# Kernel optimization log

Hardware: AMD Instinct MI355X
Metric: run time of the kernel (lower is better)

Reference implementation:

```python
import jax, jax.numpy as jnp
import numpy as np


def setup_inputs() -> dict:
    key = jax.random.key(0)
    ks = jax.random.split(key, 24)
    N, C, D_IN, HID, EMB = 8192, 4096, 32, 128, 128
    s = 0.05
    inp = {
        "cand_feat": jax.random.normal(ks[0], (1, C, D_IN), jnp.float32),
        "graph_pos": jax.random.uniform(ks[1], (N, 3), jnp.float32),
        "graph_rad": jax.random.uniform(ks[2], (N,), jnp.float32) + 0.01,
        "L": jnp.ones((1,), jnp.float32),
        "adj": jax.random.uniform(ks[3], (N, N), jnp.float32),
        "mask": jax.random.randint(ks[4], (1, C), 0, 2, jnp.int32),
        # candidate encoder: 32 -> 128 -> 128
        "cW1": jax.random.normal(ks[5], (D_IN, 128), jnp.float32) * s,
        "cb1": jnp.zeros((128,), jnp.float32),
        "cW2": jax.random.normal(ks[6], (128, EMB), jnp.float32) * s,
        "cb2": jnp.zeros((EMB,), jnp.float32),
        # graph encoder input proj: 4 -> 128
        "gW0": jax.random.normal(ks[7], (4, HID), jnp.float32) * s,
        "gb0": jnp.zeros((HID,), jnp.float32),
        # 3 GNN layers: concat(2*HID) -> HID
        "gnnW": jax.random.normal(ks[8], (3, 2 * HID, HID), jnp.float32) * s,
        "gnnb": jnp.zeros((3, HID), jnp.float32),
        # output proj: 2*HID -> EMB
        "goW": jax.random.normal(ks[9], (2 * HID, EMB), jnp.float32) * s,
        "gob": jnp.zeros((EMB,), jnp.float32),
        # fusion: 2*EMB -> 256 -> 128 -> 1
        "fW1": jax.random.normal(ks[10], (2 * EMB, 256), jnp.float32) * s,
        "fb1": jnp.zeros((256,), jnp.float32),
        "fW2": jax.random.normal(ks[11], (256, 128), jnp.float32) * s,
        "fb2": jnp.zeros((128,), jnp.float32),
        "fW3": jax.random.normal(ks[12], (128, 1), jnp.float32) * s,
        "fb3": jnp.zeros((1,), jnp.float32),
    }
    return inp


def reference(cand_feat, graph_pos, graph_rad, L, adj, mask,
              cW1, cb1, cW2, cb2, gW0, gb0, gnnW, gnnb, goW, gob,
              fW1, fb1, fW2, fb2, fW3, fb3):
    relu = jax.nn.relu
    # ---- candidate encoder: [1, C, 32] -> [1, C, 128]
    cand_emb = relu(relu(cand_feat @ cW1 + cb1) @ cW2 + cb2)
    # ---- graph encoder ----
    node = jnp.concatenate([graph_pos / L, (graph_rad / jnp.max(graph_rad))[:, None]], axis=1)  # [N, 4]
    h = relu(node @ gW0 + gb0)  # [N, HID]
    deg = jnp.clip(jnp.sum(adj, axis=-1, keepdims=True), 1.0)  # [N, 1]
    for i in range(gnnW.shape[0]):
        agg = (adj @ h) / deg                       # degree-normalized aggregation
        h = relu(jnp.concatenate([h, agg], axis=-1) @ gnnW[i] + gnnb[i])
    h_glob = jnp.concatenate([jnp.max(h, axis=0), jnp.mean(h, axis=0)], axis=-1)  # [2*HID]
    graph_emb = h_glob @ goW + gob  # [EMB]
    # ---- fusion decoder ----
    g_exp = jnp.broadcast_to(graph_emb[None, None, :], cand_emb.shape)
    combined = jnp.concatenate([cand_emb, g_exp], axis=-1)  # [1, C, 2*EMB]
    scores = (relu(relu(combined @ fW1 + fb1) @ fW2 + fb2) @ fW3 + fb3)[..., 0]  # [1, C]
    return jnp.where(mask == 0, -jnp.inf, scores)
```

## Files before the change

### kernel.cpp

```cpp
#include <hip/hip_runtime.h>
#include <hip/hip_bf16.h>

constexpr int NN  = 8192;
constexpr int CC  = 4096;
constexpr int HD  = 128;
constexpr int KSPLIT = 8;
constexpr int KCHUNK = NN / KSPLIT;
constexpr int NKP_CHUNK = KCHUNK / 64;
constexpr int NKP_TOT = NN / 64;
constexpr int CCH = 32;

typedef __attribute__((ext_vector_type(4))) float f32x4;

static __device__ __forceinline__ unsigned short f2bf(float f) {
  unsigned int u = __builtin_bit_cast(unsigned int, f);
  unsigned int lsb = (u >> 16) & 1u;
  u += 0x7fffu + lsb;
  return (unsigned short)(u >> 16);
}
static __device__ __forceinline__ float bf2f(unsigned short u) {
  return __builtin_bit_cast(float, ((unsigned int)u) << 16);
}
static __device__ __forceinline__ float e4m3f(unsigned char b) {
  unsigned e = (b >> 3) & 0xF, m = b & 7;
  if (e) return __builtin_bit_cast(float, ((e + 120u) << 23) | (m << 20));
  return (float)m * 0.001953125f;
}
static __device__ __forceinline__ unsigned long long rfl64(unsigned long long x) {
  unsigned int lo = __builtin_amdgcn_readfirstlane((unsigned int)x);
  unsigned int hi = __builtin_amdgcn_readfirstlane((unsigned int)(x >> 32));
  return ((unsigned long long)hi << 32) | lo;
}

static __device__ __forceinline__ size_t pidx8(int t16, int kbp, int lane) {
  return (((size_t)t16 * NKP_TOT + kbp) * 64 + lane) * 16;
}

__global__ __launch_bounds__(256) void k_radmax(const float* __restrict__ rad, float* out) {
  __shared__ float red[256];
  int t = threadIdx.x;
  float m = 0.0f;
  for (int i = t; i < NN; i += 256) m = fmaxf(m, rad[i]);
  red[t] = m; __syncthreads();
  for (int s = 128; s > 0; s >>= 1) {
    if (t < s) red[t] = fmaxf(red[t], red[t + s]);
    __syncthreads();
  }
  if (t == 0) out[0] = red[0];
}

__global__ __launch_bounds__(256) void k_h0(const float* __restrict__ pos, const float* __restrict__ rad,
                                            const float* __restrict__ Lp, const float* __restrict__ rmax,
                                            const float* __restrict__ gW0, const float* __restrict__ gb0,
                                            float* __restrict__ h, unsigned char* __restrict__ h8) {
  __shared__ __align__(8) unsigned char lt8[128][80];
  int t = threadIdx.x;
  int i0 = blockIdx.x * 64;
  float invL = 1.0f / Lp[0];
  float invR = 1.0f / rmax[0];
  for (int rep = 0; rep < 32; ++rep) {
    int idx = rep * 256 + t;
    int il = idx >> 7, j = idx & 127;
    int i = i0 + il;
    float n0 = pos[i * 3 + 0] * invL, n1 = pos[i * 3 + 1] * invL, n2 = pos[i * 3 + 2] * invL;
    float n3 = rad[i] * invR;
    float v = gb0[j] + n0 * gW0[j] + n1 * gW0[128 + j] + n2 * gW0[256 + j] + n3 * gW0[384 + j];
    v = fmaxf(v, 0.0f);
    h[(size_t)i * HD + j] = v;
    int enc = __builtin_amdgcn_cvt_pk_fp8_f32(v, 0.0f, 0, false);
    lt8[j][il] = (unsigned char)(enc & 0xFF);
  }
  __syncthreads();
  const int lane = t & 63, w = t >> 6;
  #pragma unroll
  for (int it = 0; it < 2; ++it) {
    int t16 = it * 4 + w;
    int j = t16 * 16 + (lane & 15);
    int ib = (lane >> 4) * 8;
    unsigned long long lo = *(const unsigned long long*)(&lt8[j][ib]);
    unsigned long long hi = *(const unsigned long long*)(&lt8[j][ib + 32]);
    uint4 q;
    q.x = (unsigned)lo; q.y = (unsigned)(lo >> 32);
    q.z = (unsigned)hi; q.w = (unsigned)(hi >> 32);
    *(uint4*)(h8 + pidx8(t16, blockIdx.x, lane)) = q;
  }
}

__global__ __launch_bounds__(256) void k_convP8(const float* __restrict__ adj,
                                                unsigned char* __restrict__ adjP8,
                                                float* __restrict__ pd) {
  __shared__ __align__(8) unsigned char lt[64 * 256];
  const int t = threadIdx.x;
  const int r0 = blockIdx.x * 64;
  const int c0 = blockIdx.y * 256;
  const int l = t & 63, w = t >> 6;
  #pragma unroll
  for (int p = 0; p < 16; ++p) {
    int r = p * 4 + w;
    int c = l * 4;
    float4 v = *(const float4*)(adj + (size_t)(r0 + r) * NN + c0 + c);
    int b32 = __builtin_amdgcn_cvt_pk_fp8_f32(v.x, v.y, 0, false);
    b32 = __builtin_amdgcn_cvt_pk_fp8_f32(v.z, v.w, b32, true);
    int g = l >> 1;
    int addr = r * 256 + ((g ^ (r & 7)) << 3) + ((l & 1) * 4);
    *(unsigned int*)(lt + addr) = (unsigned int)b32;
  }
  __syncthreads();
  {
    int r = t >> 2, qd = t & 3;
    float s = 0.f;
    #pragma unroll
    for (int k8 = 0; k8 < 8; ++k8) {
      int g = qd * 8 + k8;
      int addr = r * 256 + ((g ^ (r & 7)) << 3);
      unsigned long long v = *(const unsigned long long*)(lt + addr);
      #pragma unroll
      for (int b = 0; b < 8; ++b) s += e4m3f((unsigned char)(v >> (b * 8)));
    }
    s += __shfl_xor(s, 1);
    s += __shfl_xor(s, 2);
    if (qd == 0) pd[(size_t)blockIdx.y * NN + r0 + r] = s;
  }
  #pragma unroll
  for (int it = 0; it < 4; ++it) {
    int chunk = it * 4 + w;
    int t16l = chunk >> 2, kbpl = chunk & 3;
    int r = t16l * 16 + (l & 15);
    int cb0 = kbpl * 64 + (l >> 4) * 8;
    int g0 = cb0 >> 3, g1 = g0 + 4;
    unsigned long long lo = *(const unsigned long long*)(lt + r * 256 + ((g0 ^ (r & 7)) << 3));
    unsigned long long hi = *(const unsigned long long*)(lt + r * 256 + ((g1 ^ (r & 7)) << 3));
    uint4 q;
    q.x = (unsigned)lo; q.y = (unsigned)(lo >> 32);
    q.z = (unsigned)hi; q.w = (unsigned)(hi >> 32);
    *(uint4*)(adjP8 + pidx8(blockIdx.x * 4 + t16l, (c0 >> 6) + kbpl, l)) = q;
  }
}

__global__ __launch_bounds__(256) void k_degsum(const float* __restrict__ pd, float* __restrict__ deg) {
  int i = blockIdx.x * 256 + threadIdx.x;
  float s = 0.f;
  #pragma unroll
  for (int c = 0; c < CCH; ++c) s += pd[(size_t)c * NN + i];
  deg[i] = fmaxf(s, 1.0f);
}

#define MM32(SA_, SB_) {                                                    \
  _Pragma("unroll")                                                         \
  for (int i = 0; i < 4; ++i) {                                             \
    union { uint4 q; long long ll[2]; } ua; ua.q = SA_[i];                  \
    _Pragma("unroll")                                                       \
    for (int j = 0; j < 4; ++j) {                                           \
      union { uint4 q; long long ll[2]; } ub; ub.q = SB_[j];                \
      acc[i][j] = __builtin_amdgcn_mfma_f32_16x16x32_fp8_fp8(               \
          ua.ll[0], ub.ll[0], acc[i][j], 0, 0, 0);                          \
    } }                                                                     \
  _Pragma("unroll")                                                         \
  for (int i = 0; i < 4; ++i) {                                             \
    union { uint4 q; long long ll[2]; } ua; ua.q = SA_[i];                  \
    _Pragma("unroll")                                                       \
    for (int j = 0; j < 4; ++j) {                                           \
      union { uint4 q; long long ll[2]; } ub; ub.q = SB_[j];                \
      acc[i][j] = __builtin_amdgcn_mfma_f32_16x16x32_fp8_fp8(               \
          ua.ll[1], ub.ll[1], acc[i][j], 0, 0, 0);                          \
    } } }

#define GLD(dst, base, imm)                                               \
  asm volatile("global_load_dwordx4 %0, %1, %2 offset:" #imm              \
               : "=v"(dst) : "v"(voff), "s"(base))
#define WAITV(n) do { asm volatile("s_waitcnt vmcnt(" #n ")");            \
                      __builtin_amdgcn_sched_barrier(0); } while (0)

__global__ __launch_bounds__(256) void k_gemmP(const unsigned char* __restrict__ AP,
                                               const unsigned char* __restrict__ h8,
                                               unsigned short* __restrict__ part) {
  __shared__ __align__(16) char smem[32768];
  const int t = threadIdx.x, lane = t & 63, w = t >> 6;
  const int bm = blockIdx.x, ks = blockIdx.y;
  const int kb0p = ks * NKP_CHUNK;
  const int lr = lane & 15, kg = lane >> 4;
  const int wr = w >> 1, wc = w & 1;
  const unsigned int voff = (unsigned int)(lane * 16);

  unsigned long long bA[4], bB[4];
  #pragma unroll
  for (int q = 0; q < 4; ++q) {
    bA[q] = rfl64((unsigned long long)(AP + pidx8(bm * 8 + wr * 4 + q, kb0p, 0)));
    bB[q] = rfl64((unsigned long long)(h8 + pidx8(wc * 4 + q, kb0p, 0)));
  }

  f32x4 acc[4][4];
  #pragma unroll
  for (int i = 0; i < 4; ++i)
    #pragma unroll
    for (int j = 0; j < 4; ++j) acc[i][j] = f32x4{0.f, 0.f, 0.f, 0.f};

  uint4 S0a[4], S0b[4], S1a[4], S1b[4], S2a[4], S2b[4], S3a[4], S3b[4];

  #pragma unroll
  for (int q = 0; q < 4; ++q) { GLD(S0a[q], bA[q], 0); GLD(S0b[q], bB[q], 0); }
  #pragma unroll
  for (int q = 0; q < 4; ++q) { GLD(S1a[q], bA[q], 1024); GLD(S1b[q], bB[q], 1024); }
  #pragma unroll
  for (int q = 0; q < 4; ++q) { GLD(S2a[q], bA[q], 2048); GLD(S2b[q], bB[q], 2048); }

#define PHASE(CA, CB, NA, NB)                                             \
  do {                                                                    \
    _Pragma("unroll")                                                     \
    for (int q = 0; q < 4; ++q) { GLD(NA[q], bA[q], 3072);                \
                                  GLD(NB[q], bB[q], 3072); }              \
    _Pragma("unroll")                                                     \
    for (int q = 0; q < 4; ++q) { bA[q] += 1024; bB[q] += 1024; }         \
    WAITV(24);                                                            \
    MM32(CA, CB);                                                        \
    __builtin_amdgcn_sched_barrier(0);                                    \
  } while (0)

  for (int r = 0; r < 3; ++r) {
    PHASE(S0a, S0b, S3a, S3b);
    PHASE(S1a, S1b, S0a, S0b);
    PHASE(S2a, S2b, S1a, S1b);
    PHASE(S3a, S3b, S2a, S2b);
  }
  PHASE(S0a, S0b, S3a, S3b);
  WAITV(16);
  MM32(S1a, S1b);
  __builtin_amdgcn_sched_barrier(0);
  WAITV(8);
  MM32(S2a, S2b);
  __builtin_amdgcn_sched_barrier(0);
  WAITV(0);
  MM32(S3a, S3b);
#undef PHASE

  __syncthreads();
  unsigned short* pl = (unsigned short*)smem;
  #pragma unroll
  for (int i = 0; i < 4; ++i)
    #pragma unroll
    for (int j = 0; j < 4; ++j)
      #pragma unroll
      for (int jj = 0; jj < 4; ++jj)
        pl[(wr * 64 + i * 16 + kg * 4 + jj) * 128 + wc * 64 + j * 16 + lr] =
            f2bf(acc[i][j][jj]);
  __syncthreads();
  uint4* gout = (uint4*)(part + (size_t)ks * NN * HD + (size_t)bm * 128 * HD);
  const uint4* ls = (const uint4*)smem;
  #pragma unroll
  for (int k = 0; k < 8; ++k) gout[k * 256 + t] = ls[k * 256 + t];
}

__global__ __launch_bounds__(256) void k_update(const unsigned short* __restrict__ part,
                                                const float* __restrict__ deg,
                                                const float* __restrict__ hin,
                                                const float* __restrict__ W, const float* __restrict__ bias,
                                                float* __restrict__ hout, unsigned char* __restrict__ h8,
                                                int last) {
  __shared__ float cc[16][256];
  __shared__ __align__(8) unsigned char lt2[128][24];
  int t = threadIdx.x;
  int r0 = blockIdx.x * 16;
  for (int rep = 0; rep < 8; ++rep) {
    int idx = rep * 256 + t;
    int rl = idx >> 7, j = idx & 127;
    int row = r0 + rl;
    float s = 0.f;
    for (int ks = 0; ks < KSPLIT; ++ks)
      s += bf2f(part[((size_t)ks * NN + row) * HD + j]);
    cc[rl][128 + j] = s / deg[row];
    cc[rl][j] = hin[(size_t)row * HD + j];
  }
  __syncthreads();
  int jo = t & 127, rbase = t >> 7;
  float accv[8];
  float bj = bias[jo];
  for (int rr = 0; rr < 8; ++rr) accv[rr] = bj;
  for (int jj = 0; jj < 256; ++jj) {
    float wv = W[jj * HD + jo];
    for (int rr = 0; rr < 8; ++rr) accv[rr] += cc[rbase + rr * 2][jj] * wv;
  }
  for (int rr = 0; rr < 8; ++rr) {
    int rl = rbase + rr * 2;
    float v = fmaxf(accv[rr], 0.f);
    hout[(size_t)(r0 + rl) * HD + jo] = v;
    if (!last) {
      int enc = __builtin_amdgcn_cvt_pk_fp8_f32(v, 0.0f, 0, false);
      lt2[jo][rl] = (unsigned char)(enc & 0xFF);
    }
  }
  if (!last) {
    __syncthreads();
    const int q = (r0 >> 4) & 3;
    const int kbp = r0 >> 6;
    #pragma unroll
    for (int it = 0; it < 2; ++it) {
      int idx = it * 256 + t;
      int lane = idx & 63, t16 = (it * 256 + t) >> 6;
      int g = lane >> 4;
      if ((g >> 1) == (q & 1)) {
        int j = t16 * 16 + (lane & 15);
        unsigned long long v = *(const unsigned long long*)(&lt2[j][(g & 1) * 8]);
        *(unsigned long long*)(h8 + pidx8(t16, kbp, lane) + (q >> 1) * 8) = v;
      }
    }
  }
}

__global__ __launch_bounds__(256) void k_pool(const float* __restrict__ h,
                                              float* __restrict__ pmax, float* __restrict__ psum) {
  int b = blockIdx.x, t = threadIdx.x;
  int j = t & 127, half = t >> 7;
  int r0 = b * 128 + half * 64;
  float mx = -1e30f, sm = 0.f;
  for (int r = r0; r < r0 + 64; ++r) {
    float v = h[(size_t)r * HD + j];
    mx = fmaxf(mx, v); sm += v;
  }
  __shared__ float lm[2][128], ls[2][128];
  lm[half][j] = mx; ls[half][j] = sm;
  __syncthreads();
  if (half == 0) {
    pmax[b * 128 + j] = fmaxf(lm[0][j], lm[1][j]);
    psum[b * 128 + j] = ls[0][j] + ls[1][j];
  }
}

__global__ __launch_bounds__(256) void k_glob(const float* __restrict__ pmax, const float* __restrict__ psum,
                                              const float* __restrict__ goW, const float* __restrict__ gob,
                                              float* __restrict__ ge) {
  __shared__ float hg[256];
  int t = threadIdx.x;
  int j = t & 127, which = t >> 7;
  if (which == 0) {
    float m = -1e30f;
    for (int b = 0; b < 64; ++b) m = fmaxf(m, pmax[b * 128 + j]);
    hg[j] = m;
  } else {
    float s = 0.f;
    for (int b = 0; b < 64; ++b) s += psum[b * 128 + j];
    hg[128 + j] = s * (1.0f / (float)NN);
  }
  __syncthreads();
  if (t < 128) {
    float s = gob[t];
    for (int jj = 0; jj < 256; ++jj) s += hg[jj] * goW[jj * HD + t];
    ge[t] = s;
  }
}

__global__ __launch_bounds__(256) void k_fusion(const float* __restrict__ cand, const float* __restrict__ ge,
                                                const int* __restrict__ mask,
                                                const float* __restrict__ cW1, const float* __restrict__ cb1,
                                                const float* __restrict__ cW2, const float* __restrict__ cb2,
                                                const float* __restrict__ fW1, const float* __restrict__ fb1,
                                                const float* __restrict__ fW2, const float* __restrict__ fb2,
                                                const float* __restrict__ fW3, const float* __restrict__ fb3,
                                                float* __restrict__ out) {
  __shared__ float x[16][32];
  __shared__ float t1[16][128];
  __shared__ float t2[16][128];
  __shared__ float u1[16][256];
  __shared__ float u2[16][129];
  __shared__ float geL[128];
  int t = threadIdx.x;
  int c0 = blockIdx.x * 16;
  if (t < 128) geL[t] = ge[t];
  for (int rep = 0; rep < 2; ++rep) {
    int idx = rep * 256 + t;
    int cl = idx >> 5, d = idx & 31;
    x[cl][d] = cand[(size_t)(c0 + cl) * 32 + d];
  }
  __syncthreads();
  {
    int j = t & 127, cg = (t >> 7) * 8;
    float a[8]; float bj = cb1[j];
    for (int q = 0; q < 8; ++q) a[q] = bj;
    for (int d = 0; d < 32; ++d) {
      float wv = cW1[d * 128 + j];
      for (int q = 0; q < 8; ++q) a[q] += x[cg + q][d] * wv;
    }
    for (int q = 0; q < 8; ++q) t1[cg + q][j] = fmaxf(a[q], 0.f);
  }
  __syncthreads();
  {
    int j = t & 127, cg = (t >> 7) * 8;
    float a[8]; float bj = cb2[j];
    for (int q = 0; q < 8; ++q) a[q] = bj;
    for (int d = 0; d < 128; ++d) {
      float wv = cW2[d * 128 + j];
      for (int q = 0; q < 8; ++q) a[q] += t1[cg + q][d] * wv;
    }
    for (int q = 0; q < 8; ++q) t2[cg + q][j] = fmaxf(a[q], 0.f);
  }
  __syncthreads();
  {
    int jo = t;
    float gp = fb1[jo];
    for (int d = 0; d < 128; ++d) gp += geL[d] * fW1[(128 + d) * 256 + jo];
    float a[16];
    for (int q = 0; q < 16; ++q) a[q] = gp;
    for (int d = 0; d < 128; ++d) {
      float wv = fW1[d * 256 + jo];
      for (int q = 0; q < 16; ++q) a[q] += t2[q][d] * wv;
    }
    for (int q = 0; q < 16; ++q) u1[q][jo] = fmaxf(a[q], 0.f);
  }
  __syncthreads();
  {
    int j = t & 127, cg = (t >> 7) * 8;
    float a[8]; float bj = fb2[j];
    for (int q = 0; q < 8; ++q) a[q] = bj;
    for (int d = 0; d < 256; ++d) {
      float wv = fW2[d * 128 + j];
      for (int q = 0; q < 8; ++q) a[q] += u1[cg + q][d] * wv;
    }
    for (int q = 0; q < 8; ++q) u2[cg + q][j] = fmaxf(a[q], 0.f);
  }
  __syncthreads();
  if (t < 16) {
    int c = c0 + t;
    float s = fb3[0];
    for (int d = 0; d < 128; ++d) s += u2[t][d] * fW3[d];
    out[c] = (mask[c] == 0) ? -3.0e38f : s;
  }
}

extern "C" void kernel_launch(void* const* d_in, const int* in_sizes, int n_in,
                              void* d_out, int out_size, void* d_ws, size_t ws_size,
                              hipStream_t stream) {
  const float* cand = (const float*)d_in[0];
  const float* pos  = (const float*)d_in[1];
  const float* rad  = (const float*)d_in[2];
  const float* Lp   = (const float*)d_in[3];
  const float* adj  = (const float*)d_in[4];
  const int*   mask = (const int*)d_in[5];
  const float* cW1 = (const float*)d_in[6];
  const float* cb1 = (const float*)d_in[7];
  const float* cW2 = (const float*)d_in[8];
  const float* cb2 = (const float*)d_in[9];
  const float* gW0 = (const float*)d_in[10];
  const float* gb0 = (const float*)d_in[11];
  const float* gnnW = (const float*)d_in[12];
  const float* gnnb = (const float*)d_in[13];
  const float* goW = (const float*)d_in[14];
  const float* gob = (const float*)d_in[15];
  const float* fW1 = (const float*)d_in[16];
  const float* fb1 = (const float*)d_in[17];
  const float* fW2 = (const float*)d_in[18];
  const float* fb2 = (const float*)d_in[19];
  const float* fW3 = (const float*)d_in[20];
  const float* fb3 = (const float*)d_in[21];

  char* ws = (char*)d_ws;
  float* h            = (float*)ws;
  unsigned char* h8   = (unsigned char*)(ws + (4ull << 20));
  float* rmax         = (float*)(ws + (6ull << 20));
  float* pmax         = (float*)(ws + (6ull << 20) + 4096);
  float* psum         = pmax + 64 * 128;
  float* ge           = psum + 64 * 128;
  float* deg          = (float*)(ws + (6ull << 20) + (128u << 10));
  float* pd           = (float*)(ws + (7ull << 20));
  unsigned short* part = (unsigned short*)(ws + (8ull << 20));
  unsigned char* adjP8 = (unsigned char*)(ws + (25ull << 20));

  k_radmax<<<1, 256, 0, stream>>>(rad, rmax);
  k_h0<<<NN / 64, 256, 0, stream>>>(pos, rad, Lp, rmax, gW0, gb0, h, h8);
  {
    dim3 gc(NN / 64, CCH);
    k_convP8<<<gc, 256, 0, stream>>>(adj, adjP8, pd);
  }
  k_degsum<<<NN / 256, 256, 0, stream>>>(pd, deg);

  dim3 g(NN / 128, KSPLIT);
  for (int l = 0; l < 3; ++l) {
    k_gemmP<<<g, 256, 0, stream>>>(adjP8, h8, part);
    k_update<<<NN / 16, 256, 0, stream>>>(part, deg, h,
                                          gnnW + l * 256 * HD, gnnb + l * HD, h, h8, l == 2);
  }
  k_pool<<<64, 256, 0, stream>>>(h, pmax, psum);
  k_glob<<<1, 256, 0, stream>>>(pmax, psum, goW, gob, ge);
  k_fusion<<<CC / 16, 256, 0, stream>>>(cand, ge, mask, cW1, cb1, cW2, cb2,
                                        fW1, fb1, fW2, fb2, fW3, fb3, (float*)d_out);
}
```

Before: 354.5 us.

## Fuse first GNN layer aggregation GEMM into adjacency FP8 conversion kernel

The adjacency conversion kernel now also computes the first layer's adj@h product with FP8 MFMA on the tile it already holds in shared memory. It writes 32-way split partial sums, and k_update reduces them with a runtime ksplit argument. This removes one full pass over the FP8 adjacency and one GEMM launch. In exchange, the partial buffer grows (32 splits × N × HD bf16), k_update reads 4x more partials for layer 0, and adjP8 is moved in the workspace to make room.

```diff
diff --git a/kernel.cpp b/kernel.cpp
--- a/kernel.cpp
+++ b/kernel.cpp
@@ -5,8 +5,7 @@
 constexpr int CC  = 4096;
 constexpr int HD  = 128;
 constexpr int KSPLIT = 8;
-constexpr int KCHUNK = NN / KSPLIT;
-constexpr int NKP_CHUNK = KCHUNK / 64;
+constexpr int NKP_CHUNK = (NN / 64) / KSPLIT;
 constexpr int NKP_TOT = NN / 64;
 constexpr int CCH = 32;
 
@@ -86,10 +85,12 @@
   }
 }
 
-__global__ __launch_bounds__(256) void k_convP8(const float* __restrict__ adj,
-                                                unsigned char* __restrict__ adjP8,
-                                                float* __restrict__ pd) {
-  __shared__ __align__(8) unsigned char lt[64 * 256];
+__global__ __launch_bounds__(256) void k_convG(const float* __restrict__ adj,
+                                               const unsigned char* __restrict__ h8,
+                                               unsigned char* __restrict__ adjP8,
+                                               float* __restrict__ pd,
+                                               unsigned short* __restrict__ part) {
+  __shared__ __align__(16) unsigned char lt[64 * 256];
   const int t = threadIdx.x;
   const int r0 = blockIdx.x * 64;
   const int c0 = blockIdx.y * 256;
@@ -121,20 +122,44 @@
     s += __shfl_xor(s, 2);
     if (qd == 0) pd[(size_t)blockIdx.y * NN + r0 + r] = s;
   }
-  #pragma unroll
-  for (int it = 0; it < 4; ++it) {
-    int chunk = it * 4 + w;
-    int t16l = chunk >> 2, kbpl = chunk & 3;
-    int r = t16l * 16 + (l & 15);
-    int cb0 = kbpl * 64 + (l >> 4) * 8;
+  const int lr = l & 15, kg = l >> 4;
+  f32x4 acc[8];
+  #pragma unroll
+  for (int i = 0; i < 8; ++i) acc[i] = f32x4{0.f, 0.f, 0.f, 0.f};
+
+  #pragma unroll
+  for (int kbpl = 0; kbpl < 4; ++kbpl) {
+    int r = w * 16 + lr;
+    int cb0 = kbpl * 64 + kg * 8;
     int g0 = cb0 >> 3, g1 = g0 + 4;
-    unsigned long long lo = *(const unsigned long long*)(lt + r * 256 + ((g0 ^ (r & 7)) << 3));
-    unsigned long long hi = *(const unsigned long long*)(lt + r * 256 + ((g1 ^ (r & 7)) << 3));
+    unsigned long long alo = *(const unsigned long long*)(lt + r * 256 + ((g0 ^ (r & 7)) << 3));
+    unsigned long long ahi = *(const unsigned long long*)(lt + r * 256 + ((g1 ^ (r & 7)) << 3));
     uint4 q;
-    q.x = (unsigned)lo; q.y = (unsigned)(lo >> 32);
-    q.z = (unsigned)hi; q.w = (unsigned)(hi >> 32);
-    *(uint4*)(adjP8 + pidx8(blockIdx.x * 4 + t16l, (c0 >> 6) + kbpl, l)) = q;
-  }
+    q.x = (unsigned)alo; q.y = (unsigned)(alo >> 32);
+    q.z = (unsigned)ahi; q.w = (unsigned)(ahi >> 32);
+    *(uint4*)(adjP8 + pidx8(blockIdx.x * 4 + w, (c0 >> 6) + kbpl, l)) = q;
+    #pragma unroll
+    for (int ct = 0; ct < 8; ++ct) {
+      union { uint4 q; long long ll[2]; } ub;
+      ub.q = *(const uint4*)(h8 + pidx8(ct, (c0 >> 6) + kbpl, l));
+      acc[ct] = __builtin_amdgcn_mfma_f32_16x16x32_fp8_fp8(
+          (long long)alo, ub.ll[0], acc[ct], 0, 0, 0);
+      acc[ct] = __builtin_amdgcn_mfma_f32_16x16x32_fp8_fp8(
+          (long long)ahi, ub.ll[1], acc[ct], 0, 0, 0);
+    }
+  }
+  __syncthreads();
+  unsigned short* pl = (unsigned short*)lt;
+  #pragma unroll
+  for (int ct = 0; ct < 8; ++ct)
+    #pragma unroll
+    for (int jj = 0; jj < 4; ++jj)
+      pl[(w * 16 + kg * 4 + jj) * 128 + ct * 16 + lr] = f2bf(acc[ct][jj]);
+  __syncthreads();
+  uint4* gout = (uint4*)(part + (size_t)blockIdx.y * NN * HD + (size_t)blockIdx.x * 64 * HD);
+  const uint4* ls = (const uint4*)lt;
+  #pragma unroll
+  for (int k = 0; k < 4; ++k) gout[k * 256 + t] = ls[k * 256 + t];
 }
 
 __global__ __launch_bounds__(256) void k_degsum(const float* __restrict__ pd, float* __restrict__ deg) {
@@ -212,7 +237,7 @@
     _Pragma("unroll")                                                     \
     for (int q = 0; q < 4; ++q) { bA[q] += 1024; bB[q] += 1024; }         \
     WAITV(24);                                                            \
-    MM32(CA, CB);                                                        \
+    MM32(CA, CB);                                                         \
     __builtin_amdgcn_sched_barrier(0);                                    \
   } while (0)
 
@@ -250,7 +275,7 @@
   for (int k = 0; k < 8; ++k) gout[k * 256 + t] = ls[k * 256 + t];
 }
 
-__global__ __launch_bounds__(256) void k_update(const unsigned short* __restrict__ part,
+__global__ __launch_bounds__(256) void k_update(const unsigned short* __restrict__ part, int ksplit,
                                                 const float* __restrict__ deg,
                                                 const float* __restrict__ hin,
                                                 const float* __restrict__ W, const float* __restrict__ bias,
@@ -265,7 +290,7 @@
     int rl = idx >> 7, j = idx & 127;
     int row = r0 + rl;
     float s = 0.f;
-    for (int ks = 0; ks < KSPLIT; ++ks)
+    for (int ks = 0; ks < ksplit; ++ks)
       s += bf2f(part[((size_t)ks * NN + row) * HD + j]);
     cc[rl][128 + j] = s / deg[row];
     cc[rl][j] = hin[(size_t)row * HD + j];
@@ -461,20 +486,22 @@
   float* deg          = (float*)(ws + (6ull << 20) + (128u << 10));
   float* pd           = (float*)(ws + (7ull << 20));
   unsigned short* part = (unsigned short*)(ws + (8ull << 20));
-  unsigned char* adjP8 = (unsigned char*)(ws + (25ull << 20));
+  unsigned char* adjP8 = (unsigned char*)(ws + (73ull << 20));
 
   k_radmax<<<1, 256, 0, stream>>>(rad, rmax);
   k_h0<<<NN / 64, 256, 0, stream>>>(pos, rad, Lp, rmax, gW0, gb0, h, h8);
   {
     dim3 gc(NN / 64, CCH);
-    k_convP8<<<gc, 256, 0, stream>>>(adj, adjP8, pd);
+    k_convG<<<gc, 256, 0, stream>>>(adj, h8, adjP8, pd, part);
   }
   k_degsum<<<NN / 256, 256, 0, stream>>>(pd, deg);
+  k_update<<<NN / 16, 256, 0, stream>>>(part, CCH, deg, h,
+                                        gnnW + 0 * 256 * HD, gnnb + 0 * HD, h, h8, 0);
 
   dim3 g(NN / 128, KSPLIT);
-  for (int l = 0; l < 3; ++l) {
+  for (int l = 1; l < 3; ++l) {
     k_gemmP<<<g, 256, 0, stream>>>(adjP8, h8, part);
-    k_update<<<NN / 16, 256, 0, stream>>>(part, deg, h,
+    k_update<<<NN / 16, 256, 0, stream>>>(part, KSPLIT, deg, h,
                                           gnnW + l * 256 * HD, gnnb + l * HD, h, h8, l == 2);
   }
   k_pool<<<64, 256, 0, stream>>>(h, pmax, psum);
```

Measured after the change: 443.9 us. +25.2%, slower.
